# Kernel optimization log

Hardware: AMD Instinct MI355X
Metric: run time of the kernel (lower is better)

## Reference

```python
import jax, jax.numpy as jnp
import numpy as np


def setup_inputs() -> dict:
    key = jax.random.key(0)
    B, T, F = 128, 16384, 4
    x = jax.random.normal(key, (B, T, F), dtype=jnp.float32)
    return {"x": x, "wow": 16}


def reference(x, wow):
    # x: (B, T, F). Circular sliding-window unfold:
    # out[b, t] = concat_{k=0..wow-1} x[b, (t - wow + 1 + k) mod T, :]
    # This matches: prepend the last (wow-1) timesteps, then take every
    # length-wow window, stacked along a new axis, flattened with F.
    B, T, F = x.shape
    # idx[t, k] = (t - wow + 1 + k) mod T  -> shape (T, wow)
    idx = (jnp.arange(T)[:, None] + jnp.arange(-wow + 1, 1)[None, :]) % T
    windows = x[:, idx, :]            # (B, T, wow, F) single fused gather
    return windows.reshape(B, T, wow * F)
```

## Files before the change

kernel.cpp:

```cpp
#include <hip/hip_runtime.h>


typedef float f32x4 __attribute__((ext_vector_type(4)));

__global__ __launch_bounds__(256, 8) void ring_pad_kernel(
    const f32x4* __restrict__ x, f32x4* __restrict__ out) {
    constexpr int T    = 16384;
    constexpr int ITER = 16;
    constexpr int NWAVE = 8192;

    int lane = threadIdx.x & 63;
    int g = (blockIdx.x * blockDim.x + threadIdx.x) >> 6;

    int w  = lane & 15;
    int tl = (lane >> 4) & 3;
    int j  = lane < 31 ? lane : 30;

    #pragma unroll 2
    for (int m = 0; m < ITER; ++m) {
        int c  = m * NWAVE + g;
        int b  = c >> 10;
        int R0 = (c & 1023) << 4;

        f32x4 r = x[((size_t)b << 14) + ((R0 - 15 + j) & (T - 1))];

        f32x4* ob = out + ((size_t)c << 8);
        #pragma unroll
        for (int s = 0; s < 4; ++s) {
            int src = s * 4 + tl + w;
            f32x4 v;
            v[0] = __shfl(r[0], src, 64);
            v[1] = __shfl(r[1], src, 64);
            v[2] = __shfl(r[2], src, 64);
            v[3] = __shfl(r[3], src, 64);
            __builtin_nontemporal_store(v, &ob[s * 64 + lane]);
        }
    }
}

extern "C" void kernel_launch(void* const* d_in, const int* in_sizes, int n_in,
                              void* d_out, int out_size, void* d_ws, size_t ws_size,
                              hipStream_t stream) {
    const f32x4* x = (const f32x4*)d_in[0];
    f32x4* out = (f32x4*)d_out;

    ring_pad_kernel<<<2048, 256, 0, stream>>>(x, out);
}
```

Measured before the change: 102.1 us.

## Restructure ring-pad kernel to four-timestep waves with prefetched loads

Each wave now produces 4 timesteps (one 64-lane store) per step instead of 16 timesteps with four shuffle rounds. The wave strides through the batch dimension over 64 steps, and the next row's load is issued before the current one is shuffled and stored, giving software pipelining. This trades more loads per output (19 loaded rows per 4 outputs) for fewer shuffles per store and load latency hidden behind stores. The index arithmetic relies on hardcoded shapes and wraparound masks.

After: 119.5 us. 1.17x slower.

```diff
diff --git a/kernel.cpp b/kernel.cpp
--- a/kernel.cpp
+++ b/kernel.cpp
@@ -5,36 +5,41 @@
 
 __global__ __launch_bounds__(256, 8) void ring_pad_kernel(
     const f32x4* __restrict__ x, f32x4* __restrict__ out) {
-    constexpr int T    = 16384;
-    constexpr int ITER = 16;
-    constexpr int NWAVE = 8192;
+    constexpr int T     = 16384;
+    constexpr int STEPS = 64;
+    constexpr int XMASK = (1 << 21) - 1;
 
-    int lane = threadIdx.x & 63;
-    int g = (blockIdx.x * blockDim.x + threadIdx.x) >> 6;
+    int tid  = threadIdx.x;
+    int lane = tid & 63;
+    int g    = (((int)blockIdx.x << 8) + tid) >> 6;
 
+    int t0 = (g << 2) & (T - 1);
+    int hi = g >> 12;
+    int j  = lane < 19 ? lane : 18;
     int w  = lane & 15;
     int tl = (lane >> 4) & 3;
-    int j  = lane < 31 ? lane : 30;
+    int src = tl + w;
 
-    #pragma unroll 2
-    for (int m = 0; m < ITER; ++m) {
-        int c  = m * NWAVE + g;
-        int b  = c >> 10;
-        int R0 = (c & 1023) << 4;
+    int idx = (hi << 14) + ((t0 + T - 15 + j) & (T - 1));
 
-        f32x4 r = x[((size_t)b << 14) + ((R0 - 15 + j) & (T - 1))];
+    f32x4* op = out + ((size_t)g << 6) + lane;
 
-        f32x4* ob = out + ((size_t)c << 8);
-        #pragma unroll
-        for (int s = 0; s < 4; ++s) {
-            int src = s * 4 + tl + w;
-            f32x4 v;
-            v[0] = __shfl(r[0], src, 64);
-            v[1] = __shfl(r[1], src, 64);
-            v[2] = __shfl(r[2], src, 64);
-            v[3] = __shfl(r[3], src, 64);
-            __builtin_nontemporal_store(v, &ob[s * 64 + lane]);
-        }
+    f32x4 r = x[idx];
+    idx = (idx + (1 << 15)) & XMASK;
+
+    #pragma unroll 4
+    for (int s = 0; s < STEPS; ++s) {
+        f32x4 rn = x[idx];
+        idx = (idx + (1 << 15)) & XMASK;
+
+        f32x4 v;
+        v[0] = __shfl(r[0], src, 64);
+        v[1] = __shfl(r[1], src, 64);
+        v[2] = __shfl(r[2], src, 64);
+        v[3] = __shfl(r[3], src, 64);
+        __builtin_nontemporal_store(v, op);
+        op += (1 << 19);
+        r = rn;
     }
 }
 
```
